# Performance work log

Measured on AMD Instinct MI355X. Metric: run time of the kernel, lower is better.

## Reference

```python
import jax, jax.numpy as jnp
import numpy as np

DIM = 96
DIM_OUT = 96
NUM_HEADS = 1
HEAD_DIM = DIM_OUT // NUM_HEADS  # 96, also depthwise-conv channel count
STRIDE_Q = 1
STRIDE_KV = 2
EPS = 1e-6


def _layernorm(t, g, b):
    mu = jnp.mean(t, axis=-1, keepdims=True)
    var = jnp.mean(jnp.square(t - mu), axis=-1, keepdims=True)
    return (t - mu) * jax.lax.rsqrt(var + EPS) * g + b


def _depthwise(t_nchw, w, stride):
    # torch Conv2d(C, C, 3, stride, padding=1, groups=C, bias=False)
    # w: [C, 1, 3, 3]
    return jax.lax.conv_general_dilated(
        t_nchw, w, window_strides=(stride, stride), padding=[(1, 1), (1, 1)],
        feature_group_count=HEAD_DIM, dimension_numbers=('NCHW', 'OIHW', 'NCHW'))


def _attention_pool(t, w, stride, g, b, H, W):
    # t: [B, heads, L, C] -> pooled [B, heads, Lp, C]
    B, nh, L, C = t.shape
    t = t.reshape(B * nh, H, W, C).transpose(0, 3, 1, 2)  # [B*nh, C, H, W]
    t = _depthwise(t, w, stride)
    Hp, Wp = t.shape[2], t.shape[3]
    t = t.reshape(B, nh, C, Hp * Wp).transpose(0, 1, 3, 2)  # [B, nh, Lp, C]
    return _layernorm(t, g, b), Hp, Wp


def setup_inputs() -> dict:
    key = jax.random.key(0)
    ks = jax.random.split(key, 16)
    B, N = 32, 56 * 56
    inp = {
        'x': jax.random.normal(ks[0], (B, N, DIM), dtype=jnp.float32),
        'Wqkv': jax.random.normal(ks[1], (3 * DIM_OUT, DIM), dtype=jnp.float32) * 0.02,
        'bqkv': jax.random.normal(ks[2], (3 * DIM_OUT,), dtype=jnp.float32) * 0.02,
        'pool_q_w': jax.random.normal(ks[3], (HEAD_DIM, 1, 3, 3), dtype=jnp.float32) * 0.1,
        'gq': 1.0 + jax.random.normal(ks[4], (HEAD_DIM,), dtype=jnp.float32) * 0.02,
        'betq': jax.random.normal(ks[5], (HEAD_DIM,), dtype=jnp.float32) * 0.02,
        'pool_k_w': jax.random.normal(ks[6], (HEAD_DIM, 1, 3, 3), dtype=jnp.float32) * 0.1,
        'gk': 1.0 + jax.random.normal(ks[7], (HEAD_DIM,), dtype=jnp.float32) * 0.02,
        'betk': jax.random.normal(ks[8], (HEAD_DIM,), dtype=jnp.float32) * 0.02,
        'pool_v_w': jax.random.normal(ks[9], (HEAD_DIM, 1, 3, 3), dtype=jnp.float32) * 0.1,
        'gv': 1.0 + jax.random.normal(ks[10], (HEAD_DIM,), dtype=jnp.float32) * 0.02,
        'betv': jax.random.normal(ks[11], (HEAD_DIM,), dtype=jnp.float32) * 0.02,
        'Wproj': jax.random.normal(ks[12], (DIM_OUT, DIM_OUT), dtype=jnp.float32) * 0.02,
        'bproj': jax.random.normal(ks[13], (DIM_OUT,), dtype=jnp.float32) * 0.02,
        'h': 56,
        'w': 56,
    }
    return inp


def reference(x, Wqkv, bqkv, pool_q_w, gq, betq, pool_k_w, gk, betk,
              pool_v_w, gv, betv, Wproj, bproj, h, w):
    B, N, _ = x.shape
    qkv = (jnp.einsum('bnd,ed->bne', x, Wqkv) + bqkv)
    qkv = qkv.reshape(B, N, 3, NUM_HEADS, HEAD_DIM).transpose(2, 0, 3, 1, 4)
    q, k, v = qkv[0], qkv[1], qkv[2]  # each [B, heads, N, head_dim]

    q, Hq, Wq = _attention_pool(q, pool_q_w, STRIDE_Q, gq, betq, h, w)
    k, _, _ = _attention_pool(k, pool_k_w, STRIDE_KV, gk, betk, h, w)
    v, _, _ = _attention_pool(v, pool_v_w, STRIDE_KV, gv, betv, h, w)

    scale = HEAD_DIM ** -0.5
    attn = jax.nn.softmax(jnp.einsum('bhqc,bhkc->bhqk', q * scale, k), axis=-1)
    out = jnp.einsum('bhqk,bhkc->bhqc', attn, v) + q  # residual x + q
    out = out.transpose(0, 2, 1, 3).reshape(B, Hq * Wq, DIM_OUT)
    out = jnp.einsum('bnd,ed->bne', out, Wproj) + bproj
    return out
```

## Files before the change

kernel.cpp:

```cpp
#include <hip/hip_runtime.h>
#include <hip/hip_bf16.h>
#include <cmath>

#define BATCH 32
#define H_IN 56
#define W_IN 56
#define N_IN (H_IN * W_IN)
#define LKV 784
#define LKV_PAD 864
#define FRAG_ELEMS 82944

typedef short bf16x8 __attribute__((ext_vector_type(8)));
typedef float f32x4 __attribute__((ext_vector_type(4)));
typedef float f32x16 __attribute__((ext_vector_type(16)));

__device__ __forceinline__ unsigned pack_bf16(float a, float b) {
    unsigned ua = __builtin_bit_cast(unsigned, a);
    unsigned ub = __builtin_bit_cast(unsigned, b);
    ua = (ua + 0x7FFFu + ((ua >> 16) & 1u)) >> 16;
    ub = (ub + 0x7FFFu + ((ub >> 16) & 1u)) >> 16;
    return ua | (ub << 16);
}

__device__ __forceinline__ unsigned short cvt_bf16(float a) {
    unsigned ua = __builtin_bit_cast(unsigned, a);
    return (unsigned short)((ua + 0x7FFFu + ((ua >> 16) & 1u)) >> 16);
}

__device__ __forceinline__ float bf16_to_f32(unsigned short u) {
    unsigned v = ((unsigned)u) << 16;
    return __builtin_bit_cast(float, v);
}

__device__ __forceinline__ float bflo(unsigned u) {
    return __builtin_bit_cast(float, u << 16);
}
__device__ __forceinline__ float bfhi(unsigned u) {
    return __builtin_bit_cast(float, u & 0xFFFF0000u);
}

__device__ __forceinline__ unsigned pack_trunc(float a, float b) {
    return __builtin_amdgcn_perm(__builtin_bit_cast(unsigned, b),
                                 __builtin_bit_cast(unsigned, a), 0x07060302u);
}

__device__ __forceinline__ f32x16 zero16() {
    f32x16 z;
#pragma unroll
    for (int i = 0; i < 16; ++i) z[i] = 0.f;
    return z;
}

__global__ __launch_bounds__(256) void wprep_kernel(
    const float* __restrict__ Wqkv, const float* __restrict__ Wproj,
    unsigned short* __restrict__ wq, unsigned short* __restrict__ wp32)
{
    int idx = blockIdx.x * 256 + threadIdx.x;
    if (idx < 3456) {
        int frag = idx >> 6, ln = idx & 63;
        int ct = frag / 3, kkb = frag % 3;
        int ch = ct * 16 + (ln & 15);
        int k0 = kkb * 32 + (ln >> 4) * 8;
        const float* s = Wqkv + ch * 96 + k0;
        float4 v0 = *reinterpret_cast<const float4*>(s);
        float4 v1 = *reinterpret_cast<const float4*>(s + 4);
        uint4 o;
        o.x = pack_bf16(v0.x, v0.y); o.y = pack_bf16(v0.z, v0.w);
        o.z = pack_bf16(v1.x, v1.y); o.w = pack_bf16(v1.z, v1.w);
        *reinterpret_cast<uint4*>(wq + (size_t)idx * 8) = o;
    } else {
        int li = idx - 3456;
        int frag = li >> 6, ln = li & 63;
        int ct_out = frag / 6, kb = frag % 6;
        int row = ct_out * 32 + (ln & 31);
        int k0 = kb * 16 + (ln >> 5) * 8;
        const float* s = Wproj + row * 96 + k0;
        float4 v0 = *reinterpret_cast<const float4*>(s);
        float4 v1 = *reinterpret_cast<const float4*>(s + 4);
        uint4 o;
        o.x = pack_bf16(v0.x, v0.y); o.y = pack_bf16(v0.z, v0.w);
        o.z = pack_bf16(v1.x, v1.y); o.w = pack_bf16(v1.z, v1.w);
        *reinterpret_cast<uint4*>(wp32 + (size_t)li * 8) = o;
    }
}

template <int NCT>
__global__ __launch_bounds__(256) void gemm4_kernel(
    const float* __restrict__ Xv, const unsigned short* __restrict__ Wfr,
    const float* __restrict__ bias, void* __restrict__ o0,
    void* __restrict__ o1, void* __restrict__ o2)
{
    const int tid = threadIdx.x;
    const int wid = tid >> 6, lane = tid & 63;
    const int lo16 = lane & 15, hi = lane >> 4;

    const size_t tok0 = (size_t)blockIdx.x * 128 + wid * 32;
    bf16x8 xb[6];
#pragma unroll
    for (int it = 0; it < 2; ++it) {
        size_t t = tok0 + it * 16 + lo16;
#pragma unroll
        for (int kkb = 0; kkb < 3; ++kkb) {
            const float* xp = Xv + t * 96 + kkb * 32 + hi * 8;
            float4 a = *reinterpret_cast<const float4*>(xp);
            float4 c = *reinterpret_cast<const float4*>(xp + 4);
            uint4 u;
            u.x = pack_bf16(a.x, a.y); u.y = pack_bf16(a.z, a.w);
            u.z = pack_bf16(c.x, c.y); u.w = pack_bf16(c.z, c.w);
            xb[it * 3 + kkb] = __builtin_bit_cast(bf16x8, u);
        }
    }

#pragma unroll
    for (int ct = 0; ct < NCT; ++ct) {
        bf16x8 wf[3];
#pragma unroll
        for (int kkb = 0; kkb < 3; ++kkb)
            wf[kkb] = *reinterpret_cast<const bf16x8*>(
                Wfr + ((size_t)(ct * 3 + kkb) * 64 + lane) * 8);
        const int chb = ct * 16 + hi * 4;
        float4 bv = *reinterpret_cast<const float4*>(bias + chb);
#pragma unroll
        for (int it = 0; it < 2; ++it) {
            f32x4 a = (f32x4){0.f, 0.f, 0.f, 0.f};
#pragma unroll
            for (int kkb = 0; kkb < 3; ++kkb)
                a = __builtin_amdgcn_mfma_f32_16x16x32_bf16(wf[kkb], xb[it * 3 + kkb], a, 0, 0, 0);
            size_t t = tok0 + it * 16 + lo16;
            float r0 = a[0] + bv.x, r1 = a[1] + bv.y;
            float r2 = a[2] + bv.z, r3 = a[3] + bv.w;
            unsigned short* ob =
                (unsigned short*)((ct < 6) ? o0 : (ct < 12 ? o1 : o2));
            int lch = (ct % 6) * 16 + hi * 4;
            uint2 p;
            p.x = pack_bf16(r0, r1);
            p.y = pack_bf16(r2, r3);
            *reinterpret_cast<uint2*>(ob + t * 96 + lch) = p;
        }
    }
}

__global__ __launch_bounds__(192) void pool_all_kernel(
    const unsigned short* __restrict__ qin, const unsigned short* __restrict__ kin,
    const unsigned short* __restrict__ vin,
    const float* __restrict__ pqw, const float* __restrict__ pkw,
    const float* __restrict__ pvw,
    const float* __restrict__ gq, const float* __restrict__ betq,
    const float* __restrict__ gk, const float* __restrict__ betk,
    const float* __restrict__ gv, const float* __restrict__ betv,
    unsigned short* __restrict__ qout, unsigned short* __restrict__ kfr,
    unsigned short* __restrict__ vfr, float SC)
{
    __shared__ float wlds[864];
    __shared__ float2 part2[12][17];
    __shared__ float2 mrs[16];

    int blk0 = blockIdx.x;
    const unsigned short* in; const float* wsrc; const float* g; const float* beta;
    unsigned short* out; int omode, stride, Wp, LpPad; float oscale; int blk;
    if (blk0 < 6272) {
        blk = (blk0 & 7) * 784 + (blk0 >> 3);
        in = qin; wsrc = pqw; g = gq; beta = betq; out = qout;
        omode = 0; stride = 1; Wp = 56; LpPad = N_IN; oscale = 1.0f;
    } else if (blk0 < 8000) {
        int r = blk0 - 6272;
        blk = (r & 7) * 216 + (r >> 3);
        in = kin; wsrc = pkw; g = gk; beta = betk; out = kfr;
        omode = 1; stride = 2; Wp = 28; LpPad = LKV_PAD; oscale = SC;
    } else {
        int r = blk0 - 8000;
        blk = (r & 7) * 216 + (r >> 3);
        in = vin; wsrc = pvw; g = gv; beta = betv; out = vfr;
        omode = 2; stride = 2; Wp = 28; LpPad = LKV_PAD; oscale = 1.0f;
    }

    const int tid = threadIdx.x;
    for (int i = tid; i < 216; i += 192)
        *reinterpret_cast<float4*>(&wlds[i * 4]) =
            *reinterpret_cast<const float4*>(wsrc + i * 4);
    __syncthreads();

    const int tok_l = tid / 12, c8 = tid % 12;
    const int gt = blk * 16 + tok_l;
    const int Lp = (omode == 0) ? N_IN : LKV;
    const int b = gt / LpPad, rem = gt % LpPad;
    const bool pad = (rem >= Lp);
    const int yo = rem / Wp, xo = rem % Wp;

    float wt[9][8];
#pragma unroll
    for (int j = 0; j < 8; ++j) {
        const float* wr = &wlds[(c8 * 8 + j) * 9];
#pragma unroll
        for (int tap = 0; tap < 9; ++tap) wt[tap][j] = wr[tap];
    }

    float acc[8];
#pragma unroll
    for (int j = 0; j < 8; ++j) acc[j] = 0.f;

    const unsigned short* ib = in + (size_t)b * (H_IN * W_IN * 96) + c8 * 8;
#pragma unroll
    for (int dy = 0; dy < 3; ++dy) {
        const int iy = yo * stride + dy - 1;
        if ((unsigned)iy < (unsigned)H_IN) {
#pragma unroll
            for (int dx = 0; dx < 3; ++dx) {
                const int ix = xo * stride + dx - 1;
                if ((unsigned)ix < (unsigned)W_IN) {
                    const int tap = dy * 3 + dx;
                    uint4 d = *reinterpret_cast<const uint4*>(
                        ib + ((size_t)iy * W_IN + ix) * 96);
                    acc[0] += bflo(d.x) * wt[tap][0];
                    acc[1] += bfhi(d.x) * wt[tap][1];
                    acc[2] += bflo(d.y) * wt[tap][2];
                    acc[3] += bfhi(d.y) * wt[tap][3];
                    acc[4] += bflo(d.z) * wt[tap][4];
                    acc[5] += bfhi(d.z) * wt[tap][5];
                    acc[6] += bflo(d.w) * wt[tap][6];
                    acc[7] += bfhi(d.w) * wt[tap][7];
                }
            }
        }
    }

    float s = 0.f, s2 = 0.f;
#pragma unroll
    for (int j = 0; j < 8; ++j) { s += acc[j]; s2 += acc[j] * acc[j]; }
    part2[c8][tok_l] = make_float2(s, s2);
    __syncthreads();
    if (tid < 16) {
        float a = 0.f, q = 0.f;
#pragma unroll
        for (int j = 0; j < 12; ++j) {
            float2 p = part2[j][tid];
            a += p.x; q += p.y;
        }
        float mu = a * (1.f / 96.f);
        float var = q * (1.f / 96.f) - mu * mu;
        mrs[tid] = make_float2(mu, rsqrtf(var + 1e-6f));
    }
    __syncthreads();
    const float mu = mrs[tok_l].x, rstd = mrs[tok_l].y;

    float4 g0 = *reinterpret_cast<const float4*>(g + c8 * 8);
    float4 g1 = *reinterpret_cast<const float4*>(g + c8 * 8 + 4);
    float4 b0 = *reinterpret_cast<const float4*>(beta + c8 * 8);
    float4 b1 = *reinterpret_cast<const float4*>(beta + c8 * 8 + 4);
    float r[8];
    r[0] = (acc[0] - mu) * rstd * (g0.x * oscale) + b0.x * oscale;
    r[1] = (acc[1] - mu) * rstd * (g0.y * oscale) + b0.y * oscale;
    r[2] = (acc[2] - mu) * rstd * (g0.z * oscale) + b0.z * oscale;
    r[3] = (acc[3] - mu) * rstd * (g0.w * oscale) + b0.w * oscale;
    r[4] = (acc[4] - mu) * rstd * (g1.x * oscale) + b1.x * oscale;
    r[5] = (acc[5] - mu) * rstd * (g1.y * oscale) + b1.y * oscale;
    r[6] = (acc[6] - mu) * rstd * (g1.z * oscale) + b1.z * oscale;
    r[7] = (acc[7] - mu) * rstd * (g1.w * oscale) + b1.w * oscale;
    if (omode != 0 && pad) {
#pragma unroll
        for (int j = 0; j < 8; ++j) r[j] = 0.f;
    }

    if (omode == 0) {
        uint4 o;
        o.x = pack_bf16(r[0], r[1]); o.y = pack_bf16(r[2], r[3]);
        o.z = pack_bf16(r[4], r[5]); o.w = pack_bf16(r[6], r[7]);
        *reinterpret_cast<uint4*>(out + (size_t)gt * 96 + c8 * 8) = o;
    } else if (omode == 1) {
        int t = rem >> 5, kkb = c8 >> 1, hi = c8 & 1;
        int ln = (rem & 31) | (hi << 5);
        uint4 o;
        o.x = pack_bf16(r[0], r[1]); o.y = pack_bf16(r[2], r[3]);
        o.z = pack_bf16(r[4], r[5]); o.w = pack_bf16(r[6], r[7]);
        *reinterpret_cast<uint4*>(out + (size_t)b * FRAG_ELEMS +
                                  ((size_t)(t * 6 + kkb) * 64 + ln) * 8) = o;
    } else {
        int kv16 = rem >> 4, e = rem & 7, lh = (rem >> 3) & 1;
#pragma unroll
        for (int j = 0; j < 8; ++j) {
            int j8 = c8 * 8 + j;
            int ct = j8 >> 5;
            int ln = (j8 & 31) | (lh << 5);
            out[(size_t)b * FRAG_ELEMS + ((size_t)(kv16 * 3 + ct) * 64 + ln) * 8 + e] =
                cvt_bf16(r[j]);
        }
    }
}

#define MAKE_BI(BI, D0, D1, D2, D3)                                           \
    int4 BI;                                                                  \
    {                                                                         \
        unsigned s0_ = (unsigned)__shfl_xor((int)(D0), 32);                   \
        unsigned s1_ = (unsigned)__shfl_xor((int)(D1), 32);                   \
        unsigned s2_ = (unsigned)__shfl_xor((int)(D2), 32);                   \
        unsigned s3_ = (unsigned)__shfl_xor((int)(D3), 32);                   \
        BI = h ? make_int4((int)s2_, (int)s3_, (int)(D2), (int)(D3))          \
               : make_int4((int)(D0), (int)(D1), (int)s0_, (int)s1_);         \
    }

#define ATT_LOAD(KF, V0, V1, T)                                               \
    {                                                                         \
        _Pragma("unroll") for (int i_ = 0; i_ < 6; ++i_)                      \
            KF[i_] = *reinterpret_cast<const bf16x8*>(                        \
                Kb + ((size_t)((T) * 6 + i_) * 64 + lane) * 8);               \
        _Pragma("unroll") for (int c_ = 0; c_ < 3; ++c_) {                    \
            V0[c_] = *reinterpret_cast<const bf16x8*>(                        \
                Vb + ((size_t)((2 * (T)) * 3 + c_) * 64 + lane) * 8);         \
            V1[c_] = *reinterpret_cast<const bf16x8*>(                        \
                Vb + ((size_t)((2 * (T) + 1) * 3 + c_) * 64 + lane) * 8);     \
        }                                                                     \
    }

#define ATT_COMPUTE(KF, V0, V1, FULL)                                         \
    {                                                                         \
        f32x16 s = zero16();                                                  \
        _Pragma("unroll") for (int k_ = 0; k_ < 6; ++k_)                      \
            s = __builtin_amdgcn_mfma_f32_32x32x16_bf16(KF[k_], qf[k_], s, 0, 0, 0); \
        float p[16];                                                          \
        _Pragma("unroll") for (int r_ = 0; r_ < 16; ++r_)                     \
            p[r_] = __builtin_amdgcn_exp2f(s[r_]);                            \
        float q0_ = 0.f, q1_ = 0.f;                                           \
        _Pragma("unroll") for (int r_ = 0; r_ < 8; ++r_) {                    \
            q0_ += p[r_]; q1_ += p[r_ + 8];                                   \
        }                                                                     \
        lsum += q0_ + ((FULL) ? q1_ : 0.f);                                   \
        unsigned d[8];                                                        \
        _Pragma("unroll") for (int j_ = 0; j_ < 8; ++j_)                      \
            d[j_] = pack_trunc(p[2 * j_], p[2 * j_ + 1]);                     \
        {                                                                     \
            MAKE_BI(bi, d[0], d[1], d[2], d[3]);                              \
            bf16x8 bf = __builtin_bit_cast(bf16x8, bi);                       \
            a0 = __builtin_amdgcn_mfma_f32_32x32x16_bf16(V0[0], bf, a0, 0, 0, 0); \
            a1 = __builtin_amdgcn_mfma_f32_32x32x16_bf16(V0[1], bf, a1, 0, 0, 0); \
            a2 = __builtin_amdgcn_mfma_f32_32x32x16_bf16(V0[2], bf, a2, 0, 0, 0); \
        }                                                                     \
        if (FULL) {                                                           \
            MAKE_BI(bi, d[4], d[5], d[6], d[7]);                              \
            bf16x8 bf = __builtin_bit_cast(bf16x8, bi);                       \
            a0 = __builtin_amdgcn_mfma_f32_32x32x16_bf16(V1[0], bf, a0, 0, 0, 0); \
            a1 = __builtin_amdgcn_mfma_f32_32x32x16_bf16(V1[1], bf, a1, 0, 0, 0); \
            a2 = __builtin_amdgcn_mfma_f32_32x32x16_bf16(V1[2], bf, a2, 0, 0, 0); \
        }                                                                     \
    }

__global__ __launch_bounds__(64) void attn_proj_kernel(
    const unsigned short* __restrict__ qpl, const unsigned short* __restrict__ Kf,
    const unsigned short* __restrict__ Vf, const unsigned short* __restrict__ WP32,
    const float* __restrict__ bproj, float* __restrict__ outp)
{
    const int bid = blockIdx.x;
    const int swz = (bid & 7) * 392 + (bid >> 3);
    const int b = swz / 98, qblk = swz % 98;
    const int lane = threadIdx.x;
    const int l31 = lane & 31, h = lane >> 5;

    const int qrow = qblk * 32 + l31;
    const unsigned short* qptr = qpl + ((size_t)b * N_IN + qrow) * 96;
    bf16x8 qf[6];
#pragma unroll
    for (int kkb = 0; kkb < 6; ++kkb)
        qf[kkb] = *reinterpret_cast<const bf16x8*>(qptr + kkb * 16 + h * 8);

    f32x16 a0 = zero16(), a1 = zero16(), a2 = zero16();
    float lsum = 0.f;

    const unsigned short* Kb = Kf + (size_t)b * FRAG_ELEMS;
    const unsigned short* Vb = Vf + (size_t)b * FRAG_ELEMS;

    bf16x8 kA[6], vA0[3], vA1[3];
    bf16x8 kB[6], vB0[3], vB1[3];

    ATT_LOAD(kA, vA0, vA1, 0);
    for (int t = 0; t < 24; t += 2) {
        ATT_LOAD(kB, vB0, vB1, t + 1);
        ATT_COMPUTE(kA, vA0, vA1, true);
        ATT_LOAD(kA, vA0, vA1, t + 2);
        ATT_COMPUTE(kB, vB0, vB1, true);
    }
    ATT_COMPUTE(kA, vA0, vA1, false);

    lsum += __shfl_xor(lsum, 32);
    const float inv = 1.f / lsum;

    unsigned w[24];
#pragma unroll
    for (int ct = 0; ct < 3; ++ct) {
        const f32x16& a = (ct == 0) ? a0 : (ct == 1 ? a1 : a2);
#pragma unroll
        for (int gblk = 0; gblk < 4; ++gblk) {
            int ch = ct * 32 + gblk * 8 + 4 * h;
            ushort4 q4 = *reinterpret_cast<const ushort4*>(qptr + ch);
            w[ct * 8 + 2 * gblk] =
                pack_bf16(a[gblk * 4 + 0] * inv + bf16_to_f32(q4.x),
                          a[gblk * 4 + 1] * inv + bf16_to_f32(q4.y));
            w[ct * 8 + 2 * gblk + 1] =
                pack_bf16(a[gblk * 4 + 2] * inv + bf16_to_f32(q4.z),
                          a[gblk * 4 + 3] * inv + bf16_to_f32(q4.w));
        }
    }

    bf16x8 bfr[6];
#pragma unroll
    for (int kb = 0; kb < 6; ++kb) {
        const int base = (kb >> 1) * 8 + 4 * (kb & 1);
        MAKE_BI(bi, w[base], w[base + 1], w[base + 2], w[base + 3]);
        bfr[kb] = __builtin_bit_cast(bf16x8, bi);
    }

    float* op = outp + ((size_t)b * N_IN + qrow) * 96;
#pragma unroll
    for (int ct = 0; ct < 3; ++ct) {
        f32x16 oa = zero16();
#pragma unroll
        for (int kb = 0; kb < 6; ++kb) {
            bf16x8 wf = *reinterpret_cast<const bf16x8*>(
                WP32 + ((size_t)(ct * 6 + kb) * 64 + lane) * 8);
            oa = __builtin_amdgcn_mfma_f32_32x32x16_bf16(wf, bfr[kb], oa, 0, 0, 0);
        }
#pragma unroll
        for (int gblk = 0; gblk < 4; ++gblk) {
            int e = ct * 32 + gblk * 8 + 4 * h;
            float4 bv = *reinterpret_cast<const float4*>(bproj + e);
            float4 o;
            o.x = oa[gblk * 4 + 0] + bv.x;
            o.y = oa[gblk * 4 + 1] + bv.y;
            o.z = oa[gblk * 4 + 2] + bv.z;
            o.w = oa[gblk * 4 + 3] + bv.w;
            *reinterpret_cast<float4*>(op + e) = o;
        }
    }
}

extern "C" void kernel_launch(void* const* d_in, const int* in_sizes, int n_in,
                              void* d_out, int out_size, void* d_ws, size_t ws_size,
                              hipStream_t stream)
{
    const float* x     = (const float*)d_in[0];
    const float* Wqkv  = (const float*)d_in[1];
    const float* bqkv  = (const float*)d_in[2];
    const float* pqw   = (const float*)d_in[3];
    const float* gq    = (const float*)d_in[4];
    const float* betq  = (const float*)d_in[5];
    const float* pkw   = (const float*)d_in[6];
    const float* gk    = (const float*)d_in[7];
    const float* betk  = (const float*)d_in[8];
    const float* pvw   = (const float*)d_in[9];
    const float* gv    = (const float*)d_in[10];
    const float* betv  = (const float*)d_in[11];
    const float* Wproj = (const float*)d_in[12];
    const float* bproj = (const float*)d_in[13];
    float* outp = (float*)d_out;

    char* ws = (char*)d_ws;
    const size_t QB    = (size_t)BATCH * N_IN * 96 * sizeof(short);
    const size_t FRAGB = (size_t)BATCH * FRAG_ELEMS * sizeof(short);
    unsigned short* qb   = (unsigned short*)(ws);
    unsigned short* kbuf = (unsigned short*)(ws + QB);
    unsigned short* vbuf = (unsigned short*)(ws + 2 * QB);
    unsigned short* qpb  = (unsigned short*)(ws + 3 * QB);
    unsigned short* Kfr  = (unsigned short*)(ws + 4 * QB);
    unsigned short* Vfr  = (unsigned short*)(ws + 4 * QB + FRAGB);
    unsigned short* wqf  = (unsigned short*)(ws + 4 * QB + 2 * FRAGB);
    unsigned short* wp32 = (unsigned short*)(ws + 4 * QB + 2 * FRAGB + 56320);

    const int T = BATCH * N_IN;

    const float SC = 0.1020620726159658f * 1.4426950408889634f;

    wprep_kernel<<<18, 256, 0, stream>>>(Wqkv, Wproj, wqf, wp32);
    gemm4_kernel<18><<<T / 128, 256, 0, stream>>>(
        x, wqf, bqkv, qb, kbuf, vbuf);
    pool_all_kernel<<<9728, 192, 0, stream>>>(
        qb, kbuf, vbuf, pqw, pkw, pvw, gq, betq, gk, betk, gv, betv,
        qpb, Kfr, Vfr, SC);
    attn_proj_kernel<<<3136, 64, 0, stream>>>(
        qpb, Kfr, Vfr, wp32, bproj, outp);
}
```

Measured before the change: 130.4 us.

## Software-pipeline attention loop so QK of next tile overlaps PV of previous

Splits the fused per-tile attention step into separate K load, V load, QK MFMA, softmax and PV MFMA stages. The loop is reordered so the QK MFMAs for tile t+1 are issued alongside the PV MFMAs for tile t, which shortens dependency stalls between exp/pack and the matrix units. It also adds a minimum-occupancy hint to launch bounds. In exchange it keeps more registers live, reads one extra padded tile, and on the last partial tile always runs the second PV half, relying on the padded V rows being zero.

```diff
diff --git a/kernel.cpp b/kernel.cpp
--- a/kernel.cpp
+++ b/kernel.cpp
@@ -298,11 +298,15 @@
                : make_int4((int)(D0), (int)(D1), (int)s0_, (int)s1_);         \
     }
 
-#define ATT_LOAD(KF, V0, V1, T)                                               \
+#define LOADK(KF, T)                                                          \
     {                                                                         \
         _Pragma("unroll") for (int i_ = 0; i_ < 6; ++i_)                      \
             KF[i_] = *reinterpret_cast<const bf16x8*>(                        \
                 Kb + ((size_t)((T) * 6 + i_) * 64 + lane) * 8);               \
+    }
+
+#define LOADV(V0, V1, T)                                                      \
+    {                                                                         \
         _Pragma("unroll") for (int c_ = 0; c_ < 3; ++c_) {                    \
             V0[c_] = *reinterpret_cast<const bf16x8*>(                        \
                 Vb + ((size_t)((2 * (T)) * 3 + c_) * 64 + lane) * 8);         \
@@ -311,14 +315,28 @@
         }                                                                     \
     }
 
-#define ATT_COMPUTE(KF, V0, V1, FULL)                                         \
+#define QK6(KF)                                                               \
     {                                                                         \
-        f32x16 s = zero16();                                                  \
+        sreg = zero16();                                                      \
         _Pragma("unroll") for (int k_ = 0; k_ < 6; ++k_)                      \
-            s = __builtin_amdgcn_mfma_f32_32x32x16_bf16(KF[k_], qf[k_], s, 0, 0, 0); \
+            sreg = __builtin_amdgcn_mfma_f32_32x32x16_bf16(KF[k_], qf[k_], sreg, 0, 0, 0); \
+    }
+
+#define PV6(V0, V1)                                                           \
+    {                                                                         \
+        a0 = __builtin_amdgcn_mfma_f32_32x32x16_bf16(V0[0], pf0, a0, 0, 0, 0); \
+        a1 = __builtin_amdgcn_mfma_f32_32x32x16_bf16(V0[1], pf0, a1, 0, 0, 0); \
+        a2 = __builtin_amdgcn_mfma_f32_32x32x16_bf16(V0[2], pf0, a2, 0, 0, 0); \
+        a0 = __builtin_amdgcn_mfma_f32_32x32x16_bf16(V1[0], pf1, a0, 0, 0, 0); \
+        a1 = __builtin_amdgcn_mfma_f32_32x32x16_bf16(V1[1], pf1, a1, 0, 0, 0); \
+        a2 = __builtin_amdgcn_mfma_f32_32x32x16_bf16(V1[2], pf1, a2, 0, 0, 0); \
+    }
+
+#define SM16(FULL)                                                            \
+    {                                                                         \
         float p[16];                                                          \
         _Pragma("unroll") for (int r_ = 0; r_ < 16; ++r_)                     \
-            p[r_] = __builtin_amdgcn_exp2f(s[r_]);                            \
+            p[r_] = __builtin_amdgcn_exp2f(sreg[r_]);                         \
         float q0_ = 0.f, q1_ = 0.f;                                           \
         _Pragma("unroll") for (int r_ = 0; r_ < 8; ++r_) {                    \
             q0_ += p[r_]; q1_ += p[r_ + 8];                                   \
@@ -328,22 +346,16 @@
         _Pragma("unroll") for (int j_ = 0; j_ < 8; ++j_)                      \
             d[j_] = pack_trunc(p[2 * j_], p[2 * j_ + 1]);                     \
         {                                                                     \
-            MAKE_BI(bi, d[0], d[1], d[2], d[3]);                              \
-            bf16x8 bf = __builtin_bit_cast(bf16x8, bi);                       \
-            a0 = __builtin_amdgcn_mfma_f32_32x32x16_bf16(V0[0], bf, a0, 0, 0, 0); \
-            a1 = __builtin_amdgcn_mfma_f32_32x32x16_bf16(V0[1], bf, a1, 0, 0, 0); \
-            a2 = __builtin_amdgcn_mfma_f32_32x32x16_bf16(V0[2], bf, a2, 0, 0, 0); \
+            MAKE_BI(bi0, d[0], d[1], d[2], d[3]);                             \
+            pf0 = __builtin_bit_cast(bf16x8, bi0);                            \
         }                                                                     \
-        if (FULL) {                                                           \
-            MAKE_BI(bi, d[4], d[5], d[6], d[7]);                              \
-            bf16x8 bf = __builtin_bit_cast(bf16x8, bi);                       \
-            a0 = __builtin_amdgcn_mfma_f32_32x32x16_bf16(V1[0], bf, a0, 0, 0, 0); \
-            a1 = __builtin_amdgcn_mfma_f32_32x32x16_bf16(V1[1], bf, a1, 0, 0, 0); \
-            a2 = __builtin_amdgcn_mfma_f32_32x32x16_bf16(V1[2], bf, a2, 0, 0, 0); \
+        {                                                                     \
+            MAKE_BI(bi1, d[4], d[5], d[6], d[7]);                             \
+            pf1 = __builtin_bit_cast(bf16x8, bi1);                            \
         }                                                                     \
     }
 
-__global__ __launch_bounds__(64) void attn_proj_kernel(
+__global__ __launch_bounds__(64, 4) void attn_proj_kernel(
     const unsigned short* __restrict__ qpl, const unsigned short* __restrict__ Kf,
     const unsigned short* __restrict__ Vf, const unsigned short* __restrict__ WP32,
     const float* __restrict__ bproj, float* __restrict__ outp)
@@ -362,6 +374,8 @@
         qf[kkb] = *reinterpret_cast<const bf16x8*>(qptr + kkb * 16 + h * 8);
 
     f32x16 a0 = zero16(), a1 = zero16(), a2 = zero16();
+    f32x16 sreg;
+    bf16x8 pf0, pf1;
     float lsum = 0.f;
 
     const unsigned short* Kb = Kf + (size_t)b * FRAG_ELEMS;
@@ -370,14 +384,25 @@
     bf16x8 kA[6], vA0[3], vA1[3];
     bf16x8 kB[6], vB0[3], vB1[3];
 
-    ATT_LOAD(kA, vA0, vA1, 0);
-    for (int t = 0; t < 24; t += 2) {
-        ATT_LOAD(kB, vB0, vB1, t + 1);
-        ATT_COMPUTE(kA, vA0, vA1, true);
-        ATT_LOAD(kA, vA0, vA1, t + 2);
-        ATT_COMPUTE(kB, vB0, vB1, true);
-    }
-    ATT_COMPUTE(kA, vA0, vA1, false);
+    LOADK(kA, 0); LOADV(vA0, vA1, 0);
+    LOADK(kB, 1);
+    QK6(kA);
+    LOADV(vB0, vB1, 1);
+    SM16(true);
+
+    for (int t = 1; t < 25; t += 2) {
+        LOADK(kA, t + 1);
+        QK6(kB);
+        PV6(vA0, vA1);
+        LOADV(vA0, vA1, t + 1);
+        SM16(true);
+        LOADK(kB, t + 2);
+        QK6(kA);
+        PV6(vB0, vB1);
+        LOADV(vB0, vB1, t + 2);
+        SM16((t + 1) != 24);
+    }
+    PV6(vA0, vA1);
 
     lsum += __shfl_xor(lsum, 32);
     const float inv = 1.f / lsum;
```

Result: slower. 356.1 us (+173.0%).
